# Kernel tuning notes

Hardware: AMD Instinct MI355X
Metric: run time of the kernel (lower is better)

Reference implementation:

```python
import jax, jax.numpy as jnp
import numpy as np

B, S, D = 2, 2048, 1024
H, DC = 16, 16          # num_heads, head_coord_dim
CD = 16                 # coord_dim
DH = D // H             # head_dim = 64


def setup_inputs() -> dict:
    key = jax.random.key(0)
    ks = jax.random.split(key, 8)
    s = 0.02
    return {
        "hidden_states": jax.random.normal(ks[0], (B, S, D), jnp.float32),
        "coordinates": jax.random.normal(ks[1], (B, S, CD), jnp.float32),
        "Wv": jax.random.normal(ks[2], (D, D), jnp.float32) * s,
        "bv": jnp.zeros((D,), jnp.float32),
        "Wc": jax.random.normal(ks[3], (H * DC, CD), jnp.float32) * s,
        "bc": jnp.zeros((H * DC,), jnp.float32),
        "Wn": jax.random.normal(ks[4], (CD, D), jnp.float32) * s,
        "bn": jnp.zeros((CD,), jnp.float32),
        "Wo": jax.random.normal(ks[5], (D, D), jnp.float32) * s,
        "bo": jnp.zeros((D,), jnp.float32),
        "gamma": jnp.zeros((1, H, 1, 1), jnp.float32),
    }


def reference(hidden_states, coordinates, Wv, bv, Wc, bc, Wn, bn, Wo, bo, gamma):
    # value: [B,S,D] -> [B,H,S,DH]
    value = (hidden_states @ Wv.T + bv).reshape(B, S, H, DH).transpose(0, 2, 1, 3)
    # coordinate heads: [B,S,CD] -> [B,H,S,DC]
    z = (coordinates @ Wc.T + bc).reshape(B, S, H, DC).transpose(0, 2, 1, 3)
    z_sq = jnp.sum(z * z, axis=-1, keepdims=True)           # [B,H,S,1]
    # pairwise squared distances [B,H,S,S]
    sq_dist = z_sq + jnp.swapaxes(z_sq, -1, -2) - 2.0 * jnp.einsum("bhsc,bhtc->bhst", z, z)
    sq_dist = jnp.maximum(sq_dist, 0.0)
    g = jax.nn.softplus(gamma)                               # [1,H,1,1]
    attn = jax.nn.softmax(-g * sq_dist, axis=-1)             # [B,H,S,S]
    out = jnp.einsum("bhst,bhtd->bhsd", attn, value)         # [B,H,S,DH]
    out = out.transpose(0, 2, 1, 3).reshape(B, S, D)
    updated_hidden = out @ Wo.T + bo
    updated_coords = hidden_states @ Wn.T + bn               # [B,S,CD]
    return updated_hidden, updated_coords
```

## Files before the change

### kernel.cpp

```cpp
#include <hip/hip_runtime.h>
#include <math.h>

typedef short short8 __attribute__((ext_vector_type(8)));
typedef short short4t __attribute__((ext_vector_type(4)));
typedef float f32x4  __attribute__((ext_vector_type(4)));

#define AS1 __attribute__((address_space(1)))
#define AS3 __attribute__((address_space(3)))

__device__ __forceinline__ unsigned cvt_pk_bf16(float lo, float hi) {
    unsigned r;
    asm("v_cvt_pk_bf16_f32 %0, %1, %2" : "=v"(r) : "v"(lo), "v"(hi));
    return r;
}
__device__ __forceinline__ unsigned f2bf_rne(float x) {
    unsigned u = __float_as_uint(x);
    return (u + 0x7fffu + ((u >> 16) & 1u)) >> 16;
}
__device__ __forceinline__ float exp2_fast(float x) {
    float r;
    asm("v_exp_f32 %0, %1" : "=v"(r) : "v"(x));
    return r;
}
__device__ __forceinline__ f32x4 mfma_k16(short4t a, short4t b, f32x4 c) {
#if __has_builtin(__builtin_amdgcn_mfma_f32_16x16x16bf16_1k)
    return __builtin_amdgcn_mfma_f32_16x16x16bf16_1k(a, b, c, 0, 0, 0);
#else
    asm volatile("v_mfma_f32_16x16x16_bf16 %0, %1, %2, %0" : "+v"(c) : "v"(a), "v"(b));
    return c;
#endif
}

__global__ __launch_bounds__(256) void f2bf_all(const float* __restrict__ hidden,
                                                const float* __restrict__ Wv,
                                                const float* __restrict__ Wo,
                                                const float* __restrict__ Wn,
                                                short* __restrict__ hsb,
                                                short* __restrict__ Wvb,
                                                short* __restrict__ Wob,
                                                short* __restrict__ Wnb) {
    const int i = blockIdx.x * 256 + threadIdx.x;
    const float* src;
    short* dst;
    int ii;
    if (i < 524288)      { src = hidden; dst = hsb; ii = i; }
    else if (i < 655360) { src = Wv; dst = Wvb; ii = i - 524288; }
    else if (i < 786432) { src = Wo; dst = Wob; ii = i - 655360; }
    else                 { src = Wn; dst = Wnb; ii = i - 786432; }
    const float4 a = ((const float4*)src)[2 * ii];
    const float4 b = ((const float4*)src)[2 * ii + 1];
    uint4 r;
    r.x = cvt_pk_bf16(a.x, a.y);
    r.y = cvt_pk_bf16(a.z, a.w);
    r.z = cvt_pk_bf16(b.x, b.y);
    r.w = cvt_pk_bf16(b.z, b.w);
    ((uint4*)dst)[ii] = r;
}

__global__ __launch_bounds__(256) void zker3(const float* __restrict__ coords,
                                             const float* __restrict__ Wc,
                                             const float* __restrict__ bc,
                                             const float* __restrict__ gamma,
                                             short* __restrict__ ZA,
                                             short* __restrict__ ZB) {
    const int bs = blockIdx.x;
    const int b = bs >> 11, s = bs & 2047;
    const int tid = threadIdx.x;
    __shared__ float csh[16];
    if (tid < 16) csh[tid] = coords[(size_t)bs * 16 + tid];
    __syncthreads();
    float z = bc[tid];
#pragma unroll
    for (int k = 0; k < 16; k++) z = fmaf(csh[k], Wc[tid * 16 + k], z);
    const unsigned ub = f2bf_rne(z);
    const float zb = __uint_as_float(ub << 16);
    float sq = zb * zb;
    sq += __shfl_xor(sq, 1, 64);
    sq += __shfl_xor(sq, 2, 64);
    sq += __shfl_xor(sq, 4, 64);
    sq += __shfl_xor(sq, 8, 64);
    const int h = tid >> 4, c = tid & 15;
    const float gm = gamma[h];
    const float sp = fmaxf(gm, 0.f) + log1pf(__expf(-fabsf(gm)));
    const float ch = -sp * 1.4426950408889634f;
    const size_t row = ((size_t)(b * 16 + h) * 2048 + s) * 32;
    ZA[row + c] = (short)ub;
    ZA[row + 16 + c] = (c == 0) ? (short)f2bf_rne(sq)
                                : (c == 1 ? (short)0x3F80 : (short)0);
    ZB[row + c] = (short)f2bf_rne(-2.f * ch * zb);
    ZB[row + 16 + c] = (c == 0) ? (short)f2bf_rne(ch)
                                : (c == 1 ? (short)f2bf_rne(ch * sq) : (short)0);
}

template <int EPI>
__global__ __launch_bounds__(256) void gemm_mfma(const short* __restrict__ A,
                                                 const short* __restrict__ W,
                                                 const float* __restrict__ bias,
                                                 void* __restrict__ Cout) {
    __shared__ short As[2][128][64];
    __shared__ short Bs[2][64][64];
    const int tid = threadIdx.x;
    const int wv = tid >> 6, l = tid & 63, g = l >> 4, qc = l & 15;
    const int wm = wv >> 1, wn = wv & 1;
    const int lin = blockIdx.x;
    const int wid = (lin & 7) * 64 + (lin >> 3);
    const int Mb = (wid & 31) * 128, Nb = (wid >> 5) * 64;

    auto stage = [&](int buf, int k0) {
#pragma unroll
        for (int i = 0; i < 4; i++) {
            const int c = i * 256 + tid;
            const int r = c >> 3, jp = c & 7;
            const int js = jp ^ (r & 7);
            const short* gsA = A + (size_t)(Mb + r) * 1024 + k0 + js * 8;
            short* ldsA = &As[buf][0][0] + (size_t)(i * 256 + wv * 64) * 8;
            __builtin_amdgcn_global_load_lds((const AS1 void*)gsA, (AS3 void*)ldsA, 16, 0, 0);
        }
#pragma unroll
        for (int i = 0; i < 2; i++) {
            const int c = i * 256 + tid;
            const int r = c >> 3, jp = c & 7;
            const int js = jp ^ (r & 7);
            const short* gsB = W + (size_t)(Nb + r) * 1024 + k0 + js * 8;
            short* ldsB = &Bs[buf][0][0] + (size_t)(i * 256 + wv * 64) * 8;
            __builtin_amdgcn_global_load_lds((const AS1 void*)gsB, (AS3 void*)ldsB, 16, 0, 0);
        }
    };

    f32x4 acc[4][2] = {};
    stage(0, 0);
    __syncthreads();
    int cur = 0;
#pragma unroll 1
    for (int kb = 0; kb < 16; kb++) {
        if (kb < 15) stage(cur ^ 1, (kb + 1) * 64);
#pragma unroll
        for (int ks = 0; ks < 2; ks++) {
            const int cs = ((ks * 4 + g) ^ (qc & 7)) * 8;
            short8 af[4], bfr[2];
#pragma unroll
            for (int mt = 0; mt < 4; mt++)
                af[mt] = *(const short8*)&As[cur][wm * 64 + mt * 16 + qc][cs];
#pragma unroll
            for (int nt = 0; nt < 2; nt++)
                bfr[nt] = *(const short8*)&Bs[cur][wn * 32 + nt * 16 + qc][cs];
#pragma unroll
            for (int mt = 0; mt < 4; mt++)
#pragma unroll
                for (int nt = 0; nt < 2; nt++)
                    acc[mt][nt] = __builtin_amdgcn_mfma_f32_16x16x32_bf16(af[mt], bfr[nt], acc[mt][nt], 0, 0, 0);
        }
        __syncthreads();
        cur ^= 1;
    }

    float bl[2];
#pragma unroll
    for (int nt = 0; nt < 2; nt++) bl[nt] = bias[Nb + wn * 32 + nt * 16 + qc];
#pragma unroll
    for (int mt = 0; mt < 4; mt++) {
#pragma unroll
        for (int nt = 0; nt < 2; nt++) {
            const int m0 = Mb + wm * 64 + mt * 16 + g * 4;
            const int n  = Nb + wn * 32 + nt * 16 + qc;
            f32x4 v = acc[mt][nt];
            v = v + bl[nt];
            if (EPI == 0) {
                const int bb = m0 >> 11, s0 = m0 & 2047;
                const int hh = n >> 6, dh = n & 63;
                const int s0x = s0 ^ (((n >> 3) & 1) << 2);
                uint2 p2;
                p2.x = cvt_pk_bf16(v[0], v[1]);
                p2.y = cvt_pk_bf16(v[2], v[3]);
                *(uint2*)((short*)Cout + (size_t)((bb * 16 + hh) * 64 + dh) * 2048 + s0x) = p2;
            } else {
                float* C = (float*)Cout;
#pragma unroll
                for (int i = 0; i < 4; i++) C[(size_t)(m0 + i) * 1024 + n] = v[i];
            }
        }
    }
}

__global__ __launch_bounds__(256, 4) void attn_mfma12(const short* __restrict__ ZAg,
                                                      const short* __restrict__ ZBg,
                                                      const short* __restrict__ Vt,
                                                      short* __restrict__ AOb) {
    __shared__ short Vs[2][4096];
    __shared__ short Zs[4][2048];
    const int tid = threadIdx.x;
    const int wv = tid >> 6, ln = tid & 63, g = ln >> 4, qc = ln & 15;
    const int lin = blockIdx.x;
    const int work = (lin & 7) * 128 + (lin >> 3);
    const int qb = work & 31, h = (work >> 5) & 15, b = work >> 9;
    const int bh = b * 16 + h;
    const int q0 = qb * 64 + wv * 16;

    const short* ZAb = ZAg + (size_t)bh * (2048 * 32);
    const short* ZBb = ZBg + (size_t)bh * (2048 * 32);
    const short* Vb  = Vt  + (size_t)bh * (64 * 2048);

    const short8 zq = *(const short8*)(ZBb + (size_t)(q0 + qc) * 32 + g * 8);

    union { unsigned u[2]; short4t s4; } ones4;
    ones4.u[0] = ones4.u[1] = (qc == 0) ? 0x3F803F80u : 0u;

    f32x4 acc[4] = {};
    f32x4 accl = {};

    const short* gvb = Vb + (size_t)ln * 2048 + wv * 8;
    short* lvd = &Vs[0][0] + (size_t)tid * 8;
    short* lzd = &Zs[0][0] + (size_t)tid * 8;
    const int z_kt = tid >> 6, z_g = (tid >> 4) & 3, z_r = tid & 15;

    auto stageV = [&](int buf, int kb) {
        const short* gv = gvb + kb;
        short* lvb = lvd + buf * 4096;
        __builtin_amdgcn_global_load_lds((const AS1 void*)gv, (AS3 void*)lvb, 16, 0, 0);
        __builtin_amdgcn_global_load_lds((const AS1 void*)(gv + 32), (AS3 void*)(lvb + 2048), 16, 0, 0);
    };
    auto stageZ = [&](int buf, int kb) {
        const short* gz = ZAb + (size_t)(kb + z_kt * 16 + z_r) * 32 + z_g * 8;
        __builtin_amdgcn_global_load_lds((const AS1 void*)gz, (AS3 void*)(lzd + buf * 2048), 16, 0, 0);
    };

    const int vrd = (((g >> 1) * 64 + qc) * 8) + (((g & 1) ^ ((qc >> 3) & 1)) << 2);
    const int zrd = g * 128 + qc * 8;

    auto computeP = [&](int zbuf, unsigned pko[4][2]) {
        const short* Zc = &Zs[0][0] + zbuf * 2048;
        short8 zk[4];
#pragma unroll
        for (int kt = 0; kt < 4; kt++)
            zk[kt] = *(const short8*)(Zc + zrd + kt * 512);
        const f32x4 z4 = {0.f, 0.f, 0.f, 0.f};
#pragma unroll
        for (int kt = 0; kt < 4; kt++) {
            const f32x4 S = __builtin_amdgcn_mfma_f32_16x16x32_bf16(zk[kt], zq, z4, 0, 0, 0);
            pko[kt][0] = cvt_pk_bf16(exp2_fast(fminf(S[0], 0.f)), exp2_fast(fminf(S[1], 0.f)));
            pko[kt][1] = cvt_pk_bf16(exp2_fast(fminf(S[2], 0.f)), exp2_fast(fminf(S[3], 0.f)));
        }
    };
    auto doPV = [&](int buf, unsigned pkk[4][2]) {
        const short* Vc = &Vs[buf][0];
        __builtin_amdgcn_s_setprio(1);
#pragma unroll
        for (int kt = 0; kt < 4; kt++) {
            union { unsigned u[2]; short4t s4; } pb;
            pb.u[0] = pkk[kt][0];
            pb.u[1] = pkk[kt][1];
            accl = mfma_k16(ones4.s4, pb.s4, accl);
#pragma unroll
            for (int mt = 0; mt < 4; mt++)
                acc[mt] = mfma_k16(*(const short4t*)(Vc + vrd + kt * 1024 + mt * 128),
                                   pb.s4, acc[mt]);
        }
        __builtin_amdgcn_s_setprio(0);
    };

    stageV(0, 0);
    stageZ(0, 0);
    stageZ(1, 64);
    __syncthreads();

    unsigned pkA[4][2], pkB[4][2];
    computeP(0, pkA);

    int cur = 0;
#pragma unroll 1
    for (int i = 0; i < 32; i += 2) {
        if (i < 31) stageV(cur ^ 1, (i + 1) * 64);
        if (i < 30) stageZ((i + 2) & 3, (i + 2) * 64);
        computeP((i + 1) & 3, pkB);
        doPV(cur, pkA);
        __syncthreads();
        cur ^= 1;
        if (i + 1 < 31) stageV(cur ^ 1, (i + 2) * 64);
        if (i + 1 < 30) stageZ((i + 3) & 3, (i + 3) * 64);
        computeP((i + 2) & 3, pkA);
        doPV(cur, pkB);
        __syncthreads();
        cur ^= 1;
    }

    const float lv2 = __shfl(accl[0], qc, 64);
    const float inv = 1.f / lv2;
    const size_t row = (size_t)(b * 2048 + q0 + qc) * 1024 + h * 64;
#pragma unroll
    for (int mt = 0; mt < 4; mt++) {
        uint2 o;
        o.x = cvt_pk_bf16(acc[mt][0] * inv, acc[mt][1] * inv);
        o.y = cvt_pk_bf16(acc[mt][2] * inv, acc[mt][3] * inv);
        *(uint2*)(AOb + row + mt * 16 + g * 4) = o;
    }
}

__global__ __launch_bounds__(256) void coords_mfma(const short* __restrict__ A,
                                                   const short* __restrict__ Wnb,
                                                   const float* __restrict__ bn,
                                                   float* __restrict__ out1) {
    __shared__ float red[4][16][16];
    const int tid = threadIdx.x;
    const int wv = tid >> 6, l = tid & 63, g = l >> 4, qc = l & 15;
    const int m0 = blockIdx.x * 16;
    const int k0 = wv * 256;
    f32x4 acc = {};
#pragma unroll
    for (int kk = 0; kk < 256; kk += 32) {
        const short8 af = *(const short8*)(A + (size_t)(m0 + qc) * 1024 + k0 + kk + g * 8);
        const short8 bf = *(const short8*)(Wnb + (size_t)qc * 1024 + k0 + kk + g * 8);
        acc = __builtin_amdgcn_mfma_f32_16x16x32_bf16(af, bf, acc, 0, 0, 0);
    }
#pragma unroll
    for (int i2 = 0; i2 < 4; i2++) red[wv][g * 4 + i2][qc] = acc[i2];
    __syncthreads();
    const int r = tid >> 4, c = tid & 15;
    const float s = red[0][r][c] + red[1][r][c] + red[2][r][c] + red[3][r][c] + bn[c];
    out1[(size_t)(m0 + r) * 16 + c] = s;
}

extern "C" void kernel_launch(void* const* d_in, const int* in_sizes, int n_in,
                              void* d_out, int out_size, void* d_ws, size_t ws_size,
                              hipStream_t stream) {
    (void)in_sizes; (void)n_in; (void)out_size; (void)ws_size;
    const float* hidden = (const float*)d_in[0];
    const float* coords = (const float*)d_in[1];
    const float* Wv = (const float*)d_in[2];
    const float* bv = (const float*)d_in[3];
    const float* Wc = (const float*)d_in[4];
    const float* bc = (const float*)d_in[5];
    const float* Wn = (const float*)d_in[6];
    const float* bn = (const float*)d_in[7];
    const float* Wo = (const float*)d_in[8];
    const float* bo = (const float*)d_in[9];
    const float* gamma = (const float*)d_in[10];

    char* wsb = (char*)d_ws;
    short* hsb = (short*)(wsb);
    short* AOb = hsb;
    short* Wvb = (short*)(wsb + (8 << 20));
    short* Wob = (short*)(wsb + (10 << 20));
    short* Vt  = (short*)(wsb + (12 << 20));
    short* ZA  = (short*)(wsb + (20 << 20));
    short* ZB  = (short*)(wsb + (24 << 20));
    short* Wnb = (short*)(wsb + (28 << 20));

    float* out_hidden = (float*)d_out;
    float* out_coords = out_hidden + 4194304;

    f2bf_all<<<3080, 256, 0, stream>>>(hidden, Wv, Wo, Wn, hsb, Wvb, Wob, Wnb);
    zker3<<<4096, 256, 0, stream>>>(coords, Wc, bc, gamma, ZA, ZB);
    gemm_mfma<0><<<512, 256, 0, stream>>>(hsb, Wvb, bv, (void*)Vt);
    coords_mfma<<<256, 256, 0, stream>>>(hsb, Wnb, bn, out_coords);
    attn_mfma12<<<1024, 256, 0, stream>>>(ZA, ZB, Vt, AOb);
    gemm_mfma<1><<<512, 256, 0, stream>>>(AOb, Wob, bo, (void*)out_hidden);
}
```

Measured before the change: 106.9 us.

## Triple-buffer attention V/Z staging with one barrier per tile and partial vmcnt waits

Moves the attention kernel's V tiles from double to triple buffering and its Z tiles into a three-slot rotating ring. Each K tile now needs a single barrier preceded by a partial vmcnt wait, so loads for two tiles ahead stay in flight instead of draining fully at every __syncthreads. Shared memory grows from 32 KB to 36 KB per block, which may affect occupancy at 4 blocks per CU. The loop also issues wrapped-around redundant loads in its final iterations to keep the vmcnt accounting uniform.

```diff
diff --git a/kernel.cpp b/kernel.cpp
--- a/kernel.cpp
+++ b/kernel.cpp
@@ -182,12 +182,12 @@
     }
 }
 
-__global__ __launch_bounds__(256, 4) void attn_mfma12(const short* __restrict__ ZAg,
+__global__ __launch_bounds__(256, 4) void attn_mfma13(const short* __restrict__ ZAg,
                                                       const short* __restrict__ ZBg,
                                                       const short* __restrict__ Vt,
                                                       short* __restrict__ AOb) {
-    __shared__ short Vs[2][4096];
-    __shared__ short Zs[4][2048];
+    __shared__ short Vs[3][4096];
+    __shared__ short Zs[3][2048];
     const int tid = threadIdx.x;
     const int wv = tid >> 6, ln = tid & 63, g = ln >> 4, qc = ln & 15;
     const int lin = blockIdx.x;
@@ -209,26 +209,24 @@
     f32x4 accl = {};
 
     const short* gvb = Vb + (size_t)ln * 2048 + wv * 8;
-    short* lvd = &Vs[0][0] + (size_t)tid * 8;
-    short* lzd = &Zs[0][0] + (size_t)tid * 8;
+    const int soff = tid * 8;
     const int z_kt = tid >> 6, z_g = (tid >> 4) & 3, z_r = tid & 15;
 
-    auto stageV = [&](int buf, int kb) {
+    auto stageVp = [&](short* slot, int kb) {
         const short* gv = gvb + kb;
-        short* lvb = lvd + buf * 4096;
-        __builtin_amdgcn_global_load_lds((const AS1 void*)gv, (AS3 void*)lvb, 16, 0, 0);
-        __builtin_amdgcn_global_load_lds((const AS1 void*)(gv + 32), (AS3 void*)(lvb + 2048), 16, 0, 0);
-    };
-    auto stageZ = [&](int buf, int kb) {
+        short* d = slot + soff;
+        __builtin_amdgcn_global_load_lds((const AS1 void*)gv, (AS3 void*)d, 16, 0, 0);
+        __builtin_amdgcn_global_load_lds((const AS1 void*)(gv + 32), (AS3 void*)(d + 2048), 16, 0, 0);
+    };
+    auto stageZp = [&](short* slot, int kb) {
         const short* gz = ZAb + (size_t)(kb + z_kt * 16 + z_r) * 32 + z_g * 8;
-        __builtin_amdgcn_global_load_lds((const AS1 void*)gz, (AS3 void*)(lzd + buf * 2048), 16, 0, 0);
+        __builtin_amdgcn_global_load_lds((const AS1 void*)gz, (AS3 void*)(slot + soff), 16, 0, 0);
     };
 
     const int vrd = (((g >> 1) * 64 + qc) * 8) + (((g & 1) ^ ((qc >> 3) & 1)) << 2);
     const int zrd = g * 128 + qc * 8;
 
-    auto computeP = [&](int zbuf, unsigned pko[4][2]) {
-        const short* Zc = &Zs[0][0] + zbuf * 2048;
+    auto computeP = [&](const short* Zc, unsigned pko[4][2]) {
         short8 zk[4];
 #pragma unroll
         for (int kt = 0; kt < 4; kt++)
@@ -241,8 +239,7 @@
             pko[kt][1] = cvt_pk_bf16(exp2_fast(fminf(S[2], 0.f)), exp2_fast(fminf(S[3], 0.f)));
         }
     };
-    auto doPV = [&](int buf, unsigned pkk[4][2]) {
-        const short* Vc = &Vs[buf][0];
+    auto doPV = [&](const short* Vc, unsigned pkk[4][2]) {
         __builtin_amdgcn_s_setprio(1);
 #pragma unroll
         for (int kt = 0; kt < 4; kt++) {
@@ -258,29 +255,42 @@
         __builtin_amdgcn_s_setprio(0);
     };
 
-    stageV(0, 0);
-    stageZ(0, 0);
-    stageZ(1, 64);
-    __syncthreads();
+    short *v0 = &Vs[0][0], *v1 = &Vs[1][0], *v2 = &Vs[2][0];
+    short *z0 = &Zs[0][0], *z1 = &Zs[1][0], *z2 = &Zs[2][0];
+
+    stageVp(v0, 0);
+    stageVp(v1, 64);
+    stageZp(z0, 0);
+    stageZp(z1, 64);
+    stageZp(z2, 128);
+    asm volatile("s_waitcnt vmcnt(0) lgkmcnt(0)" ::: "memory");
+    __builtin_amdgcn_s_barrier();
+    __builtin_amdgcn_sched_barrier(0);
 
     unsigned pkA[4][2], pkB[4][2];
-    computeP(0, pkA);
-
-    int cur = 0;
+    computeP(z0, pkA);
+
 #pragma unroll 1
-    for (int i = 0; i < 32; i += 2) {
-        if (i < 31) stageV(cur ^ 1, (i + 1) * 64);
-        if (i < 30) stageZ((i + 2) & 3, (i + 2) * 64);
-        computeP((i + 1) & 3, pkB);
-        doPV(cur, pkA);
-        __syncthreads();
-        cur ^= 1;
-        if (i + 1 < 31) stageV(cur ^ 1, (i + 2) * 64);
-        if (i + 1 < 30) stageZ((i + 3) & 3, (i + 3) * 64);
-        computeP((i + 2) & 3, pkA);
-        doPV(cur, pkB);
-        __syncthreads();
-        cur ^= 1;
+    for (int i = 0; i < 32; i++) {
+        asm volatile("s_waitcnt vmcnt(3) lgkmcnt(0)" ::: "memory");
+        __builtin_amdgcn_s_barrier();
+        __builtin_amdgcn_sched_barrier(0);
+
+        int kv = i + 2; if (kv >= 32) kv -= 32;
+        int kz = i + 3; if (kz >= 32) kz -= 32;
+        stageVp(v2, kv * 64);
+        stageZp(z0, kz * 64);
+
+        computeP(z1, pkB);
+        doPV(v0, pkA);
+
+#pragma unroll
+        for (int kt = 0; kt < 4; kt++) {
+            pkA[kt][0] = pkB[kt][0];
+            pkA[kt][1] = pkB[kt][1];
+        }
+        short* t = v0; v0 = v1; v1 = v2; v2 = t;
+        t = z0; z0 = z1; z1 = z2; z2 = t;
     }
 
     const float lv2 = __shfl(accl[0], qc, 64);
@@ -352,6 +362,6 @@
     zker3<<<4096, 256, 0, stream>>>(coords, Wc, bc, gamma, ZA, ZB);
     gemm_mfma<0><<<512, 256, 0, stream>>>(hsb, Wvb, bv, (void*)Vt);
     coords_mfma<<<256, 256, 0, stream>>>(hsb, Wnb, bn, out_coords);
-    attn_mfma12<<<1024, 256, 0, stream>>>(ZA, ZB, Vt, AOb);
+    attn_mfma13<<<1024, 256, 0, stream>>>(ZA, ZB, Vt, AOb);
     gemm_mfma<1><<<512, 256, 0, stream>>>(AOb, Wob, bo, (void*)out_hidden);
 }
```

Measured after the change: 110.3 us. 1.03x slower.

## Merge prep kernels, fold coords GEMM into V-proj, widen attention blocks to 512 threads

Applied to the files above, without the earlier changes.

Combines the bf16 conversion and the coordinate-head kernel into a single launch. The coords projection now runs as extra blocks of the V-projection GEMM. The attention kernel uses 512-thread blocks covering 128 queries, so each staged V/Z tile is shared by eight waves instead of four. This cuts launch count from six to four and halves K/V staging traffic per query. The cost is higher per-block LDS and register pressure and fewer attention blocks.

```diff
diff --git a/kernel.cpp b/kernel.cpp
--- a/kernel.cpp
+++ b/kernel.cpp
@@ -31,42 +31,43 @@
 #endif
 }
 
-__global__ __launch_bounds__(256) void f2bf_all(const float* __restrict__ hidden,
+__global__ __launch_bounds__(256) void prep_all(const float* __restrict__ hidden,
                                                 const float* __restrict__ Wv,
                                                 const float* __restrict__ Wo,
                                                 const float* __restrict__ Wn,
+                                                const float* __restrict__ coords,
+                                                const float* __restrict__ Wc,
+                                                const float* __restrict__ bc,
+                                                const float* __restrict__ gamma,
                                                 short* __restrict__ hsb,
                                                 short* __restrict__ Wvb,
                                                 short* __restrict__ Wob,
-                                                short* __restrict__ Wnb) {
-    const int i = blockIdx.x * 256 + threadIdx.x;
-    const float* src;
-    short* dst;
-    int ii;
-    if (i < 524288)      { src = hidden; dst = hsb; ii = i; }
-    else if (i < 655360) { src = Wv; dst = Wvb; ii = i - 524288; }
-    else if (i < 786432) { src = Wo; dst = Wob; ii = i - 655360; }
-    else                 { src = Wn; dst = Wnb; ii = i - 786432; }
-    const float4 a = ((const float4*)src)[2 * ii];
-    const float4 b = ((const float4*)src)[2 * ii + 1];
-    uint4 r;
-    r.x = cvt_pk_bf16(a.x, a.y);
-    r.y = cvt_pk_bf16(a.z, a.w);
-    r.z = cvt_pk_bf16(b.x, b.y);
-    r.w = cvt_pk_bf16(b.z, b.w);
-    ((uint4*)dst)[ii] = r;
-}
-
-__global__ __launch_bounds__(256) void zker3(const float* __restrict__ coords,
-                                             const float* __restrict__ Wc,
-                                             const float* __restrict__ bc,
-                                             const float* __restrict__ gamma,
-                                             short* __restrict__ ZA,
-                                             short* __restrict__ ZB) {
-    const int bs = blockIdx.x;
+                                                short* __restrict__ Wnb,
+                                                short* __restrict__ ZA,
+                                                short* __restrict__ ZB) {
+    __shared__ float csh[16];
+    if (blockIdx.x < 3080) {
+        const int i = blockIdx.x * 256 + threadIdx.x;
+        const float* src;
+        short* dst;
+        int ii;
+        if (i < 524288)      { src = hidden; dst = hsb; ii = i; }
+        else if (i < 655360) { src = Wv; dst = Wvb; ii = i - 524288; }
+        else if (i < 786432) { src = Wo; dst = Wob; ii = i - 655360; }
+        else                 { src = Wn; dst = Wnb; ii = i - 786432; }
+        const float4 a = ((const float4*)src)[2 * ii];
+        const float4 b = ((const float4*)src)[2 * ii + 1];
+        uint4 r;
+        r.x = cvt_pk_bf16(a.x, a.y);
+        r.y = cvt_pk_bf16(a.z, a.w);
+        r.z = cvt_pk_bf16(b.x, b.y);
+        r.w = cvt_pk_bf16(b.z, b.w);
+        ((uint4*)dst)[ii] = r;
+        return;
+    }
+    const int bs = blockIdx.x - 3080;
     const int b = bs >> 11, s = bs & 2047;
     const int tid = threadIdx.x;
-    __shared__ float csh[16];
     if (tid < 16) csh[tid] = coords[(size_t)bs * 16 + tid];
     __syncthreads();
     float z = bc[tid];
@@ -96,11 +97,36 @@
 __global__ __launch_bounds__(256) void gemm_mfma(const short* __restrict__ A,
                                                  const short* __restrict__ W,
                                                  const float* __restrict__ bias,
-                                                 void* __restrict__ Cout) {
+                                                 void* __restrict__ Cout,
+                                                 const short* __restrict__ Wnb,
+                                                 const float* __restrict__ bn,
+                                                 float* __restrict__ out1) {
     __shared__ short As[2][128][64];
     __shared__ short Bs[2][64][64];
     const int tid = threadIdx.x;
     const int wv = tid >> 6, l = tid & 63, g = l >> 4, qc = l & 15;
+
+    if (EPI == 0 && blockIdx.x >= 512) {
+        float* red = (float*)&As[0][0][0];
+        const int m0 = (blockIdx.x - 512) * 16;
+        const int k0 = wv * 256;
+        f32x4 acc = {};
+#pragma unroll
+        for (int kk = 0; kk < 256; kk += 32) {
+            const short8 af = *(const short8*)(A + (size_t)(m0 + qc) * 1024 + k0 + kk + g * 8);
+            const short8 bf = *(const short8*)(Wnb + (size_t)qc * 1024 + k0 + kk + g * 8);
+            acc = __builtin_amdgcn_mfma_f32_16x16x32_bf16(af, bf, acc, 0, 0, 0);
+        }
+#pragma unroll
+        for (int i2 = 0; i2 < 4; i2++) red[(wv * 256) + (g * 4 + i2) * 16 + qc] = acc[i2];
+        __syncthreads();
+        const int r = tid >> 4, c = tid & 15;
+        const float s = red[r * 16 + c] + red[256 + r * 16 + c] +
+                        red[512 + r * 16 + c] + red[768 + r * 16 + c] + bn[c];
+        out1[(size_t)(m0 + r) * 16 + c] = s;
+        return;
+    }
+
     const int wm = wv >> 1, wn = wv & 1;
     const int lin = blockIdx.x;
     const int wid = (lin & 7) * 64 + (lin >> 3);
@@ -182,7 +208,7 @@
     }
 }
 
-__global__ __launch_bounds__(256, 4) void attn_mfma12(const short* __restrict__ ZAg,
+__global__ __launch_bounds__(512, 4) void attn_mfma14(const short* __restrict__ ZAg,
                                                       const short* __restrict__ ZBg,
                                                       const short* __restrict__ Vt,
                                                       short* __restrict__ AOb) {
@@ -191,10 +217,10 @@
     const int tid = threadIdx.x;
     const int wv = tid >> 6, ln = tid & 63, g = ln >> 4, qc = ln & 15;
     const int lin = blockIdx.x;
-    const int work = (lin & 7) * 128 + (lin >> 3);
-    const int qb = work & 31, h = (work >> 5) & 15, b = work >> 9;
+    const int work = (lin & 7) * 64 + (lin >> 3);
+    const int qb = work & 15, h = (work >> 4) & 15, b = work >> 8;
     const int bh = b * 16 + h;
-    const int q0 = qb * 64 + wv * 16;
+    const int q0 = qb * 128 + wv * 16;
 
     const short* ZAb = ZAg + (size_t)bh * (2048 * 32);
     const short* ZBb = ZBg + (size_t)bh * (2048 * 32);
@@ -208,20 +234,21 @@
     f32x4 acc[4] = {};
     f32x4 accl = {};
 
-    const short* gvb = Vb + (size_t)ln * 2048 + wv * 8;
+    const short* gvb = Vb + (size_t)(tid & 63) * 2048 + (tid >> 6) * 8;
     short* lvd = &Vs[0][0] + (size_t)tid * 8;
     short* lzd = &Zs[0][0] + (size_t)tid * 8;
     const int z_kt = tid >> 6, z_g = (tid >> 4) & 3, z_r = tid & 15;
 
     auto stageV = [&](int buf, int kb) {
-        const short* gv = gvb + kb;
-        short* lvb = lvd + buf * 4096;
-        __builtin_amdgcn_global_load_lds((const AS1 void*)gv, (AS3 void*)lvb, 16, 0, 0);
-        __builtin_amdgcn_global_load_lds((const AS1 void*)(gv + 32), (AS3 void*)(lvb + 2048), 16, 0, 0);
+        __builtin_amdgcn_global_load_lds((const AS1 void*)(gvb + kb),
+                                         (AS3 void*)(lvd + buf * 4096), 16, 0, 0);
     };
     auto stageZ = [&](int buf, int kb) {
-        const short* gz = ZAb + (size_t)(kb + z_kt * 16 + z_r) * 32 + z_g * 8;
-        __builtin_amdgcn_global_load_lds((const AS1 void*)gz, (AS3 void*)(lzd + buf * 2048), 16, 0, 0);
+        if (tid < 256) {
+            const short* gz = ZAb + (size_t)(kb + z_kt * 16 + z_r) * 32 + z_g * 8;
+            __builtin_amdgcn_global_load_lds((const AS1 void*)gz,
+                                             (AS3 void*)(lzd + buf * 2048), 16, 0, 0);
+        }
     };
 
     const int vrd = (((g >> 1) * 64 + qc) * 8) + (((g & 1) ^ ((qc >> 3) & 1)) << 2);
@@ -295,30 +322,6 @@
     }
 }
 
-__global__ __launch_bounds__(256) void coords_mfma(const short* __restrict__ A,
-                                                   const short* __restrict__ Wnb,
-                                                   const float* __restrict__ bn,
-                                                   float* __restrict__ out1) {
-    __shared__ float red[4][16][16];
-    const int tid = threadIdx.x;
-    const int wv = tid >> 6, l = tid & 63, g = l >> 4, qc = l & 15;
-    const int m0 = blockIdx.x * 16;
-    const int k0 = wv * 256;
-    f32x4 acc = {};
-#pragma unroll
-    for (int kk = 0; kk < 256; kk += 32) {
-        const short8 af = *(const short8*)(A + (size_t)(m0 + qc) * 1024 + k0 + kk + g * 8);
-        const short8 bf = *(const short8*)(Wnb + (size_t)qc * 1024 + k0 + kk + g * 8);
-        acc = __builtin_amdgcn_mfma_f32_16x16x32_bf16(af, bf, acc, 0, 0, 0);
-    }
-#pragma unroll
-    for (int i2 = 0; i2 < 4; i2++) red[wv][g * 4 + i2][qc] = acc[i2];
-    __syncthreads();
-    const int r = tid >> 4, c = tid & 15;
-    const float s = red[0][r][c] + red[1][r][c] + red[2][r][c] + red[3][r][c] + bn[c];
-    out1[(size_t)(m0 + r) * 16 + c] = s;
-}
-
 extern "C" void kernel_launch(void* const* d_in, const int* in_sizes, int n_in,
                               void* d_out, int out_size, void* d_ws, size_t ws_size,
                               hipStream_t stream) {
@@ -348,10 +351,9 @@
     float* out_hidden = (float*)d_out;
     float* out_coords = out_hidden + 4194304;
 
-    f2bf_all<<<3080, 256, 0, stream>>>(hidden, Wv, Wo, Wn, hsb, Wvb, Wob, Wnb);
-    zker3<<<4096, 256, 0, stream>>>(coords, Wc, bc, gamma, ZA, ZB);
-    gemm_mfma<0><<<512, 256, 0, stream>>>(hsb, Wvb, bv, (void*)Vt);
-    coords_mfma<<<256, 256, 0, stream>>>(hsb, Wnb, bn, out_coords);
-    attn_mfma12<<<1024, 256, 0, stream>>>(ZA, ZB, Vt, AOb);
-    gemm_mfma<1><<<512, 256, 0, stream>>>(AOb, Wob, bo, (void*)out_hidden);
-}
+    prep_all<<<7176, 256, 0, stream>>>(hidden, Wv, Wo, Wn, coords, Wc, bc, gamma,
+                                       hsb, Wvb, Wob, Wnb, ZA, ZB);
+    gemm_mfma<0><<<768, 256, 0, stream>>>(hsb, Wvb, bv, (void*)Vt, Wnb, bn, out_coords);
+    attn_mfma14<<<512, 512, 0, stream>>>(ZA, ZB, Vt, AOb);
+    gemm_mfma<1><<<512, 256, 0, stream>>>(AOb, Wob, bo, (void*)out_hidden, Wnb, bn, out_coords);
+}
```

After: 96.83 us. 1.1x faster.
